# Performance work log

Hardware: AMD Instinct MI355X
Metric: run time of the kernel (lower is better)

## Reference

```python
import jax, jax.numpy as jnp
import numpy as np

B, K, D_MODEL = 64, 256, 512
D_STATE, D_CONV, EXPAND = 16, 4, 1
D_INNER = EXPAND * D_MODEL
DT_RANK = (D_MODEL + 15) // 16  # 32
EPS = 1e-5


def _layer_norm(x, g, b):
    m = jnp.mean(x, axis=-1, keepdims=True)
    v = jnp.mean(jnp.square(x - m), axis=-1, keepdims=True)
    return (x - m) * jax.lax.rsqrt(v + EPS) * g + b


def _silu(x):
    return x * jax.nn.sigmoid(x)


def _mamba_block(x, in_proj_w, conv_w, conv_b, x_proj_w, dt_proj_w, dt_proj_b, A_log, Dp, out_proj_w):
    # x: (B, K, d_model)
    b, k, _ = x.shape
    d_inner = A_log.shape[0]
    d_state = A_log.shape[1]
    dt_rank = dt_proj_w.shape[1]
    xz = x @ in_proj_w.T                      # (B, K, 2*d_inner)
    xi, z = jnp.split(xz, 2, axis=-1)
    # causal depthwise conv1d, width d_conv
    pad = conv_w.shape[1] - 1
    xp = jnp.pad(xi, ((0, 0), (pad, 0), (0, 0)))
    xc = conv_b + sum(xp[:, w:w + k, :] * conv_w[:, w] for w in range(conv_w.shape[1]))
    xc = _silu(xc)
    proj = xc @ x_proj_w.T                    # (B, K, dt_rank + 2*d_state)
    dtr = proj[..., :dt_rank]
    Bc = proj[..., dt_rank:dt_rank + d_state]  # (B, K, d_state)
    Cc = proj[..., dt_rank + d_state:]         # (B, K, d_state)
    dt = jax.nn.softplus(dtr @ dt_proj_w.T + dt_proj_b)  # (B, K, d_inner)
    A = -jnp.exp(A_log)                       # (d_inner, d_state)

    def step(h, inp):
        dt_t, x_t, B_t, C_t = inp             # (B,d_inner),(B,d_inner),(B,d_state),(B,d_state)
        dA = jnp.exp(dt_t[:, :, None] * A)    # (B, d_inner, d_state)
        h = dA * h + (dt_t * x_t)[:, :, None] * B_t[:, None, :]
        y = jnp.einsum('bds,bs->bd', h, C_t)
        return h, y

    h0 = jnp.zeros((b, d_inner, d_state), x.dtype)
    xs = (dt.transpose(1, 0, 2), xc.transpose(1, 0, 2),
          Bc.transpose(1, 0, 2), Cc.transpose(1, 0, 2))
    _, ys = jax.lax.scan(step, h0, xs)        # ys: (K, B, d_inner)
    y = ys.transpose(1, 0, 2) + xc * Dp       # skip term D*x
    y = y * _silu(z)
    return y @ out_proj_w.T


def setup_inputs() -> dict:
    key = jax.random.key(0)
    ks = jax.random.split(key, 8)
    s = 0.02
    slots = jax.random.normal(ks[0], (B, K, D_MODEL), dtype=jnp.float32)
    in_proj_w = jax.random.normal(ks[1], (2 * D_INNER, D_MODEL), jnp.float32) * s
    conv_w = jax.random.normal(ks[2], (D_INNER, D_CONV), jnp.float32) * 0.1
    conv_b = jnp.zeros((D_INNER,), jnp.float32)
    x_proj_w = jax.random.normal(ks[3], (DT_RANK + 2 * D_STATE, D_INNER), jnp.float32) * s
    dt_proj_w = jax.random.normal(ks[4], (D_INNER, DT_RANK), jnp.float32) * s
    dt_proj_b = jax.random.normal(ks[5], (D_INNER,), jnp.float32) * 0.1 - 4.0  # small softplus(dt)
    A_log = jnp.log(jnp.broadcast_to(jnp.arange(1, D_STATE + 1, dtype=jnp.float32), (D_INNER, D_STATE)))
    Dp = jnp.ones((D_INNER,), jnp.float32)
    out_proj_w = jax.random.normal(ks[6], (D_MODEL, D_INNER), jnp.float32) * s
    ln_g = jnp.ones((D_MODEL,), jnp.float32)
    ln_b = jnp.zeros((D_MODEL,), jnp.float32)
    fln_g = jnp.ones((D_MODEL,), jnp.float32)
    fln_b = jnp.zeros((D_MODEL,), jnp.float32)
    return {"slots": slots, "ln_g": ln_g, "ln_b": ln_b,
            "in_proj_w": in_proj_w, "conv_w": conv_w, "conv_b": conv_b,
            "x_proj_w": x_proj_w, "dt_proj_w": dt_proj_w, "dt_proj_b": dt_proj_b,
            "A_log": A_log, "Dp": Dp, "out_proj_w": out_proj_w,
            "fln_g": fln_g, "fln_b": fln_b}


def reference(slots, ln_g, ln_b, in_proj_w, conv_w, conv_b, x_proj_w,
              dt_proj_w, dt_proj_b, A_log, Dp, out_proj_w, fln_g, fln_b):
    x = slots
    # num_layers = 1: pre-norm -> mamba -> residual
    residual = x
    x = _layer_norm(x, ln_g, ln_b)
    x = _mamba_block(x, in_proj_w, conv_w, conv_b, x_proj_w,
                     dt_proj_w, dt_proj_b, A_log, Dp, out_proj_w)
    x = x + residual
    return _layer_norm(x, fln_g, fln_b)
```

## Files before the change

kernel.cpp:

```cpp
#include <hip/hip_runtime.h>
#include <hip/hip_bf16.h>


#define NTOK 16384
#define DM   512

typedef __attribute__((ext_vector_type(8))) short bf16x8;
typedef __attribute__((ext_vector_type(4))) float f32x4;

__device__ __forceinline__ unsigned short f2bf(float f){
  unsigned int u = __float_as_uint(f);
  u = (u + 0x7fffu + ((u >> 16) & 1u)) >> 16;
  return (unsigned short)u;
}
__device__ __forceinline__ float bfu(unsigned short p){ return __uint_as_float(((unsigned int)p) << 16); }
__device__ __forceinline__ unsigned int pk2(float a, float b){
  return (unsigned int)f2bf(a) | ((unsigned int)f2bf(b) << 16);
}
__device__ __forceinline__ float silu(float a){ return a / (1.f + __expf(-a)); }

__device__ __forceinline__ void async_cp16(const unsigned short* g, unsigned short* l){
  __builtin_amdgcn_global_load_lds(
      (const __attribute__((address_space(1))) unsigned int*)g,
      (__attribute__((address_space(3))) unsigned int*)l, 16, 0, 0);
}

__global__ __launch_bounds__(256) void k_cvtw(const float* __restrict__ W,
                                              unsigned short* __restrict__ Wb){
  int i = (blockIdx.x*256 + threadIdx.x)*8;
  float4 a = *(const float4*)(W+i);
  float4 b = *(const float4*)(W+i+4);
  uint4 st = { pk2(a.x,a.y), pk2(a.z,a.w), pk2(b.x,b.y), pk2(b.z,b.w) };
  *(uint4*)(Wb+i) = st;
}

__global__ __launch_bounds__(64) void k_ln(const float* __restrict__ x,
                                           const float* __restrict__ g,
                                           const float* __restrict__ b,
                                           unsigned short* __restrict__ out){
  int tok  = blockIdx.x;
  int lane = threadIdx.x;
  const float* row = x + (size_t)tok*DM + lane*8;
  float4 r0 = *(const float4*)row;
  float4 r1 = *(const float4*)(row + 4);
  float v[8] = {r0.x,r0.y,r0.z,r0.w, r1.x,r1.y,r1.z,r1.w};
  float s = 0.f;
  #pragma unroll
  for (int i=0;i<8;i++) s += v[i];
  #pragma unroll
  for (int o=32;o;o>>=1) s += __shfl_xor(s, o, 64);
  float m = s * (1.0f/512.0f);
  float vs = 0.f;
  #pragma unroll
  for (int i=0;i<8;i++){ float d = v[i]-m; vs += d*d; }
  #pragma unroll
  for (int o=32;o;o>>=1) vs += __shfl_xor(vs, o, 64);
  float rs = rsqrtf(vs*(1.0f/512.0f) + 1e-5f);
  float4 g0 = *(const float4*)(g + lane*8);
  float4 g1 = *(const float4*)(g + lane*8 + 4);
  float4 b0 = *(const float4*)(b + lane*8);
  float4 b1 = *(const float4*)(b + lane*8 + 4);
  float gv[8] = {g0.x,g0.y,g0.z,g0.w, g1.x,g1.y,g1.z,g1.w};
  float bv[8] = {b0.x,b0.y,b0.z,b0.w, b1.x,b1.y,b1.z,b1.w};
  float o8[8];
  #pragma unroll
  for (int i=0;i<8;i++) o8[i] = (v[i]-m)*rs*gv[i] + bv[i];
  uint4 st = { pk2(o8[0],o8[1]), pk2(o8[2],o8[3]), pk2(o8[4],o8[5]), pk2(o8[6],o8[7]) };
  *(uint4*)(out + (size_t)tok*DM + lane*8) = st;
}

__global__ __launch_bounds__(256) void k_gemm(const unsigned short* __restrict__ A,
                                              const unsigned short* __restrict__ Wb,
                                              float* __restrict__ out_f,
                                              unsigned short* __restrict__ out_b,
                                              int mode){
  __shared__ unsigned short As[2][128*32];
  __shared__ unsigned short Bs[2][128*32];
  int t0  = blockIdx.x * 128;
  int n0  = blockIdx.y * 128;
  int tid = threadIdx.x;
  int lane = tid & 63;
  int wv  = tid >> 6;
  int mw  = wv & 1, nw = wv >> 1;
  int m15 = lane & 15, quad = lane >> 4;

  int srow   = wv*32 + (lane >> 2);
  int schunk = ((lane & 3) ^ ((lane >> 3) & 3)) * 8;
  const unsigned short* gA = A  + (size_t)(t0 + srow)*DM + schunk;
  const unsigned short* gB = Wb + (size_t)(n0 + srow)*DM + schunk;
  unsigned short* asb0 = &As[0][(wv*32)*32];
  unsigned short* bsb0 = &Bs[0][(wv*32)*32];
  unsigned short* asb1 = &As[1][(wv*32)*32];
  unsigned short* bsb1 = &Bs[1][(wv*32)*32];

  async_cp16(gA,         asb0);
  async_cp16(gA + 16*DM, asb0 + 16*32);
  async_cp16(gB,         bsb0);
  async_cp16(gB + 16*DM, bsb0 + 16*32);

  f32x4 acc[4][4];
  #pragma unroll
  for (int rb=0;rb<4;rb++)
    #pragma unroll
    for (int cb=0;cb<4;cb++) acc[rb][cb] = (f32x4){0.f,0.f,0.f,0.f};

  int rdsw = (quad ^ ((m15 >> 1) & 3)) * 8;
  int cur = 0;
  for (int ks = 0; ks < 16; ks++){
    __syncthreads();
    if (ks < 15){
      const unsigned short* nA = gA + (ks+1)*32;
      const unsigned short* nB = gB + (ks+1)*32;
      unsigned short* na = cur ? asb0 : asb1;
      unsigned short* nb = cur ? bsb0 : bsb1;
      async_cp16(nA,         na);
      async_cp16(nA + 16*DM, na + 16*32);
      async_cp16(nB,         nb);
      async_cp16(nB + 16*DM, nb + 16*32);
    }
    bf16x8 af[4], bfr[4];
    #pragma unroll
    for (int rb=0;rb<4;rb++)
      af[rb] = *(const bf16x8*)&As[cur][(mw*64 + rb*16 + m15)*32 + rdsw];
    #pragma unroll
    for (int cb=0;cb<4;cb++)
      bfr[cb] = *(const bf16x8*)&Bs[cur][(nw*64 + cb*16 + m15)*32 + rdsw];
    #pragma unroll
    for (int rb=0;rb<4;rb++)
      #pragma unroll
      for (int cb=0;cb<4;cb++)
        acc[rb][cb] = __builtin_amdgcn_mfma_f32_16x16x32_bf16(af[rb], bfr[cb], acc[rb][cb], 0, 0, 0);
    cur ^= 1;
  }

  #pragma unroll
  for (int rb=0;rb<4;rb++){
    int tok0 = t0 + mw*64 + rb*16 + quad*4;
    int b    = tok0 >> 8;
    int tl0  = tok0 & 255;
    #pragma unroll
    for (int cb=0;cb<4;cb++){
      int nn = n0 + nw*64 + cb*16 + m15;
      f32x4 v = acc[rb][cb];
      if (mode == 0){
        if (nn < DM){
          *(f32x4*)(out_f + ((size_t)(b*DM + nn))*256 + tl0) = v;
        } else {
          uint2 z2 = { pk2(silu(v[0]), silu(v[1])), pk2(silu(v[2]), silu(v[3])) };
          *(uint2*)(out_b + ((size_t)(b*DM + (nn - DM)))*256 + tl0) = z2;
        }
      } else {
        #pragma unroll
        for (int r=0;r<4;r++) out_f[(size_t)(tok0+r)*DM + nn] = v[r];
      }
    }
  }
}

__global__ __launch_bounds__(256) void k_xproj(const float* __restrict__ xiT,
                                               const float* __restrict__ cw,
                                               const float* __restrict__ cb,
                                               const unsigned short* __restrict__ xpwb,
                                               const unsigned short* __restrict__ dtwb,
                                               const float* __restrict__ dtb,
                                               float* __restrict__ dtT,
                                               float* __restrict__ Bc,
                                               float* __restrict__ Cc){
  __shared__ unsigned short xcb[32*520];
  __shared__ unsigned short Bst[2][64*32];
  __shared__ unsigned short pjA[32*40];
  int t0  = blockIdx.x * 32;
  int b   = t0 >> 8;
  int tl0 = t0 & 255;
  int tid = threadIdx.x;
  int lane = tid & 63;
  int wv  = tid >> 6;
  int m15 = lane & 15, quad = lane >> 4;

  #pragma unroll
  for (int j=0;j<2;j++){
    int d = tid + 256*j;
    float4 cr = *(const float4*)(cw + d*4);
    float a0 = cb[d];
    const float* row = xiT + ((size_t)(b*DM + d))*256;
    float w[36];
    if (tl0 == 0){
      w[0]=w[1]=w[2]=w[3]=0.f;
      #pragma unroll
      for (int q2=0;q2<8;q2++){
        float4 v4 = *(const float4*)(row + q2*4);
        w[4+q2*4]=v4.x; w[5+q2*4]=v4.y; w[6+q2*4]=v4.z; w[7+q2*4]=v4.w;
      }
    } else {
      const float* p4 = row + tl0 - 4;
      #pragma unroll
      for (int q2=0;q2<9;q2++){
        float4 v4 = *(const float4*)(p4 + q2*4);
        w[q2*4]=v4.x; w[1+q2*4]=v4.y; w[2+q2*4]=v4.z; w[3+q2*4]=v4.w;
      }
    }
    #pragma unroll
    for (int t=0;t<32;t++){
      float a = a0 + w[t+1]*cr.x + w[t+2]*cr.y + w[t+3]*cr.z + w[t+4]*cr.w;
      xcb[t*520 + d] = f2bf(silu(a));
    }
  }

  int srow = wv*16 + (lane >> 2);
  int sch  = ((lane & 3) ^ ((lane >> 3) & 3)) * 8;
  async_cp16(xpwb + srow*DM + sch, &Bst[0][(wv*16)*32]);
  __syncthreads();

  int mt = wv & 1, ntp = wv >> 1;
  f32x4 pacc[2];
  pacc[0] = (f32x4){0.f,0.f,0.f,0.f};
  pacc[1] = (f32x4){0.f,0.f,0.f,0.f};
  int rdsw = (quad ^ ((m15 >> 1) & 3)) * 8;
  int cur = 0;
  for (int ks=0; ks<16; ks++){
    if (ks < 15)
      async_cp16(xpwb + srow*DM + (ks+1)*32 + sch, &Bst[cur^1][(wv*16)*32]);
    bf16x8 af = *(const bf16x8*)&xcb[(mt*16 + m15)*520 + ks*32 + quad*8];
    #pragma unroll
    for (int j2=0;j2<2;j2++){
      int nt = ntp*2 + j2;
      bf16x8 bfr = *(const bf16x8*)&Bst[cur][(nt*16 + m15)*32 + rdsw];
      pacc[j2] = __builtin_amdgcn_mfma_f32_16x16x32_bf16(af, bfr, pacc[j2], 0, 0, 0);
    }
    cur ^= 1;
    __syncthreads();
  }

  if (ntp == 0){
    #pragma unroll
    for (int j2=0;j2<2;j2++){
      int col = j2*16 + m15;
      #pragma unroll
      for (int r=0;r<4;r++)
        pjA[(mt*16 + quad*4 + r)*40 + col] = f2bf(pacc[j2][r]);
    }
  } else {
    #pragma unroll
    for (int j2=0;j2<2;j2++){
      int c = j2*16 + m15;
      #pragma unroll
      for (int r=0;r<4;r++){
        int tt = t0 + mt*16 + quad*4 + r;
        float v = pacc[j2][r];
        if (c < 16) Bc[(size_t)tt*16 + c] = v;
        else        Cc[(size_t)tt*16 + (c-16)] = v;
      }
    }
  }
  __syncthreads();

  bf16x8 adt = *(const bf16x8*)&pjA[(mt*16 + m15)*40 + quad*8];
  int nh = wv >> 1;
  #pragma unroll
  for (int j2=0;j2<16;j2++){
    int nn = (nh*16 + j2)*16 + m15;
    bf16x8 bfr = *(const bf16x8*)(dtwb + nn*32 + quad*8);
    f32x4 dacc = (f32x4){0.f,0.f,0.f,0.f};
    dacc = __builtin_amdgcn_mfma_f32_16x16x32_bf16(adt, bfr, dacc, 0, 0, 0);
    float bb = dtb[nn];
    f32x4 o;
    #pragma unroll
    for (int r=0;r<4;r++){
      float s = dacc[r] + bb;
      o[r] = (s > 20.f) ? s : log1pf(__expf(s));
    }
    *(f32x4*)(dtT + ((size_t)(b*DM + nn))*256 + tl0 + mt*16 + quad*4) = o;
  }
}

__global__ __launch_bounds__(256) void k_scan(const float* __restrict__ dtT,
                                              const float* __restrict__ xiT,
                                              const unsigned short* __restrict__ zsT,
                                              const float* __restrict__ Bc,
                                              const float* __restrict__ Cc,
                                              const float* __restrict__ cw,
                                              const float* __restrict__ cb,
                                              const float* __restrict__ Alog,
                                              const float* __restrict__ Dpw,
                                              unsigned short* __restrict__ ya){
  int tid = threadIdx.x;
  int sl  = tid & 3;
  int q   = blockIdx.x*64 + (tid >> 2);
  int d   = q & 511;
  int b   = q >> 9;
  float4 Alr = *(const float4*)(Alog + d*16 + sl*4);
  float A0 = -__expf(Alr.x), A1 = -__expf(Alr.y);
  float A2 = -__expf(Alr.z), A3 = -__expf(Alr.w);
  float Dv = Dpw[d];
  float4 cr = *(const float4*)(cw + d*4);
  float cbv = cb[d];
  float h0=0.f, h1=0.f, h2=0.f, h3=0.f;
  float xm1=0.f, xm2=0.f, xm3=0.f;
  const float* dtp = dtT + (size_t)q*256;
  const float* xip = xiT + (size_t)q*256;
  const unsigned short* zsp = zsT + (size_t)q*256;
  unsigned short* yap = ya + (size_t)b*256*DM + d;
  const float* Bp = Bc + (size_t)b*4096 + sl*4;
  const float* Cp = Cc + (size_t)b*4096 + sl*4;
  #pragma unroll 2
  for (int t0=0; t0<256; t0+=4){
    float4 dt4 = *(const float4*)(dtp + t0);
    float4 xi4 = *(const float4*)(xip + t0);
    uint2  zz  = *(const uint2*)(zsp + t0);
    float xts[4] = {xi4.x, xi4.y, xi4.z, xi4.w};
    float dvs[4] = {dt4.x, dt4.y, dt4.z, dt4.w};
    float zsf[4] = { bfu((unsigned short)zz.x), bfu((unsigned short)(zz.x>>16)),
                     bfu((unsigned short)zz.y), bfu((unsigned short)(zz.y>>16)) };
    #pragma unroll
    for (int r=0;r<4;r++){
      float4 Bv = *(const float4*)(Bp + (t0+r)*16);
      float4 Cv = *(const float4*)(Cp + (t0+r)*16);
      float a  = cbv + xm3*cr.x + xm2*cr.y + xm1*cr.z + xts[r]*cr.w;
      float u  = silu(a);
      float dv = dvs[r];
      float du = dv*u;
      h0 = __expf(dv*A0)*h0 + du*Bv.x;
      h1 = __expf(dv*A1)*h1 + du*Bv.y;
      h2 = __expf(dv*A2)*h2 + du*Bv.z;
      h3 = __expf(dv*A3)*h3 + du*Bv.w;
      float yy = h0*Cv.x + h1*Cv.y + h2*Cv.z + h3*Cv.w;
      yy += __shfl_xor(yy, 1);
      yy += __shfl_xor(yy, 2);
      if (sl == 0) yap[(size_t)(t0+r)*DM] = f2bf((yy + u*Dv) * zsf[r]);
      xm3 = xm2; xm2 = xm1; xm1 = xts[r];
    }
  }
}

__global__ __launch_bounds__(64) void k_fln(const float* __restrict__ o,
                                            const float* __restrict__ resid,
                                            const float* __restrict__ g,
                                            const float* __restrict__ b,
                                            float* __restrict__ out){
  int tok  = blockIdx.x;
  int lane = threadIdx.x;
  const float* row = o     + (size_t)tok*DM + lane*8;
  const float* rr  = resid + (size_t)tok*DM + lane*8;
  float4 r0 = *(const float4*)row;
  float4 r1 = *(const float4*)(row + 4);
  float4 s0 = *(const float4*)rr;
  float4 s1 = *(const float4*)(rr + 4);
  float v[8] = {r0.x+s0.x, r0.y+s0.y, r0.z+s0.z, r0.w+s0.w,
                r1.x+s1.x, r1.y+s1.y, r1.z+s1.z, r1.w+s1.w};
  float s = 0.f;
  #pragma unroll
  for (int i=0;i<8;i++) s += v[i];
  #pragma unroll
  for (int o2=32;o2;o2>>=1) s += __shfl_xor(s, o2, 64);
  float m = s * (1.0f/512.0f);
  float vs = 0.f;
  #pragma unroll
  for (int i=0;i<8;i++){ float d = v[i]-m; vs += d*d; }
  #pragma unroll
  for (int o2=32;o2;o2>>=1) vs += __shfl_xor(vs, o2, 64);
  float rs = rsqrtf(vs*(1.0f/512.0f) + 1e-5f);
  float4 g0 = *(const float4*)(g + lane*8);
  float4 g1 = *(const float4*)(g + lane*8 + 4);
  float4 b0 = *(const float4*)(b + lane*8);
  float4 b1 = *(const float4*)(b + lane*8 + 4);
  float gv[8] = {g0.x,g0.y,g0.z,g0.w, g1.x,g1.y,g1.z,g1.w};
  float bv[8] = {b0.x,b0.y,b0.z,b0.w, b1.x,b1.y,b1.z,b1.w};
  float o8[8];
  #pragma unroll
  for (int i=0;i<8;i++) o8[i] = (v[i]-m)*rs*gv[i] + bv[i];
  float4* op = (float4*)(out + (size_t)tok*DM + lane*8);
  op[0] = make_float4(o8[0],o8[1],o8[2],o8[3]);
  op[1] = make_float4(o8[4],o8[5],o8[6],o8[7]);
}

extern "C" void kernel_launch(void* const* d_in, const int* in_sizes, int n_in,
                              void* d_out, int out_size, void* d_ws, size_t ws_size,
                              hipStream_t stream) {
  const float* slots     = (const float*)d_in[0];
  const float* ln_g      = (const float*)d_in[1];
  const float* ln_b      = (const float*)d_in[2];
  const float* in_proj_w = (const float*)d_in[3];
  const float* conv_w    = (const float*)d_in[4];
  const float* conv_b    = (const float*)d_in[5];
  const float* x_proj_w  = (const float*)d_in[6];
  const float* dt_proj_w = (const float*)d_in[7];
  const float* dt_proj_b = (const float*)d_in[8];
  const float* A_log     = (const float*)d_in[9];
  const float* Dp        = (const float*)d_in[10];
  const float* out_projw = (const float*)d_in[11];
  const float* fln_g     = (const float*)d_in[12];
  const float* fln_b     = (const float*)d_in[13];
  float* out = (float*)d_out;

  const size_t MB = 1024*1024;
  char* base = (char*)d_ws;
  float*          xiT  = (float*)(base);
  unsigned short* xlnb = (unsigned short*)(base + 32*MB);
  unsigned short* yab  = xlnb;
  unsigned short* xpwb = xlnb;
  unsigned short* dtwb = xlnb + 32768;
  unsigned short* zsT  = (unsigned short*)(base + 48*MB);
  unsigned short* WbO  = zsT;
  float*          dto  = (float*)(base + 64*MB);
  unsigned short* WbI  = (unsigned short*)dto;
  float*          Bc   = (float*)(base + 96*MB);
  float*          Cc   = (float*)(base + 97*MB);

  k_ln   <<<NTOK,           64, 0, stream>>>(slots, ln_g, ln_b, xlnb);
  k_cvtw <<<256,           256, 0, stream>>>(in_proj_w, WbI);
  k_gemm <<<dim3(128, 8),  256, 0, stream>>>(xlnb, WbI, xiT, zsT, 0);
  k_cvtw <<<16,            256, 0, stream>>>(x_proj_w, xpwb);
  k_cvtw <<<8,             256, 0, stream>>>(dt_proj_w, dtwb);
  k_xproj<<<NTOK/32,       256, 0, stream>>>(xiT, conv_w, conv_b, xpwb, dtwb, dt_proj_b,
                                             dto, Bc, Cc);
  k_scan <<<512,           256, 0, stream>>>(dto, xiT, zsT, Bc, Cc, conv_w, conv_b, A_log, Dp, yab);
  k_cvtw <<<128,           256, 0, stream>>>(out_projw, WbO);
  k_gemm <<<dim3(128, 4),  256, 0, stream>>>(yab, WbO, dto, (unsigned short*)0, 1);
  k_fln  <<<NTOK,           64, 0, stream>>>(dto, slots, fln_g, fln_b, out);
}
```

Baseline: 319.6 us.

## Split selective scan into chunked three-pass parallel scan over time

```diff
diff --git a/kernel.cpp b/kernel.cpp
--- a/kernel.cpp
+++ b/kernel.cpp
@@ -18,6 +18,9 @@
   return (unsigned int)f2bf(a) | ((unsigned int)f2bf(b) << 16);
 }
 __device__ __forceinline__ float silu(float a){ return a / (1.f + __expf(-a)); }
+__device__ __forceinline__ float silu_f(float a){
+  return a * __builtin_amdgcn_rcpf(1.f + __expf(-a));
+}
 
 __device__ __forceinline__ void async_cp16(const unsigned short* g, unsigned short* l){
   __builtin_amdgcn_global_load_lds(
@@ -202,7 +205,7 @@
     #pragma unroll
     for (int t=0;t<32;t++){
       float a = a0 + w[t+1]*cr.x + w[t+2]*cr.y + w[t+3]*cr.z + w[t+4]*cr.w;
-      xcb[t*520 + d] = f2bf(silu(a));
+      xcb[t*520 + d] = f2bf(silu_f(a));
     }
   }
 
@@ -273,37 +276,114 @@
   }
 }
 
-__global__ __launch_bounds__(256) void k_scan(const float* __restrict__ dtT,
-                                              const float* __restrict__ xiT,
-                                              const unsigned short* __restrict__ zsT,
-                                              const float* __restrict__ Bc,
-                                              const float* __restrict__ Cc,
-                                              const float* __restrict__ cw,
-                                              const float* __restrict__ cb,
-                                              const float* __restrict__ Alog,
-                                              const float* __restrict__ Dpw,
-                                              unsigned short* __restrict__ ya){
+__global__ __launch_bounds__(256) void k_scan1(const float* __restrict__ dtT,
+                                               const float* __restrict__ xiT,
+                                               const float* __restrict__ Bc,
+                                               const float* __restrict__ cw,
+                                               const float* __restrict__ cb,
+                                               const float* __restrict__ Alog,
+                                               float* __restrict__ PL){
   int tid = threadIdx.x;
   int sl  = tid & 3;
-  int q   = blockIdx.x*64 + (tid >> 2);
+  int blk = blockIdx.x;
+  int c   = blk & 3;
+  int q   = (blk >> 2)*64 + (tid >> 2);
   int d   = q & 511;
   int b   = q >> 9;
+  int tl0 = c*64;
+  float4 Alr = *(const float4*)(Alog + d*16 + sl*4);
+  float A0 = -__expf(Alr.x), A1 = -__expf(Alr.y);
+  float A2 = -__expf(Alr.z), A3 = -__expf(Alr.w);
+  float4 cr = *(const float4*)(cw + d*4);
+  float cbv = cb[d];
+  const float* dtp = dtT + (size_t)q*256;
+  const float* xip = xiT + (size_t)q*256;
+  const float* Bp  = Bc + (size_t)b*4096 + sl*4;
+  float xm1, xm2, xm3;
+  if (c == 0){ xm1 = xm2 = xm3 = 0.f; }
+  else { float4 xw = *(const float4*)(xip + tl0 - 4); xm3 = xw.y; xm2 = xw.z; xm1 = xw.w; }
+  float h0=0.f,h1=0.f,h2=0.f,h3=0.f;
+  float p0=1.f,p1=1.f,p2=1.f,p3=1.f;
+  #pragma unroll 2
+  for (int t0=tl0; t0<tl0+64; t0+=4){
+    float4 dt4 = *(const float4*)(dtp + t0);
+    float4 xi4 = *(const float4*)(xip + t0);
+    float xts[4] = {xi4.x, xi4.y, xi4.z, xi4.w};
+    float dvs[4] = {dt4.x, dt4.y, dt4.z, dt4.w};
+    #pragma unroll
+    for (int r=0;r<4;r++){
+      float4 Bv = *(const float4*)(Bp + (t0+r)*16);
+      float a  = cbv + xm3*cr.x + xm2*cr.y + xm1*cr.z + xts[r]*cr.w;
+      float u  = silu_f(a);
+      float dv = dvs[r];
+      float du = dv*u;
+      float e0 = __expf(dv*A0), e1 = __expf(dv*A1);
+      float e2 = __expf(dv*A2), e3 = __expf(dv*A3);
+      h0 = e0*h0 + du*Bv.x;  p0 *= e0;
+      h1 = e1*h1 + du*Bv.y;  p1 *= e1;
+      h2 = e2*h2 + du*Bv.z;  p2 *= e2;
+      h3 = e3*h3 + du*Bv.w;  p3 *= e3;
+      xm3 = xm2; xm2 = xm1; xm1 = xts[r];
+    }
+  }
+  float* p = PL + (((size_t)q*4 + c)*32 + sl*8);
+  *(f32x4*)p       = (f32x4){p0,p1,p2,p3};
+  *(f32x4*)(p + 4) = (f32x4){h0,h1,h2,h3};
+}
+
+__global__ __launch_bounds__(256) void k_scan2(const float* __restrict__ PL,
+                                               float* __restrict__ h0buf){
+  int i = blockIdx.x*256 + threadIdx.x;
+  int q = i >> 2, sl = i & 3;
+  const float* p = PL + ((size_t)q*4)*32 + sl*8;
+  f32x4 h = (f32x4){0.f,0.f,0.f,0.f};
+  #pragma unroll
+  for (int c=0;c<4;c++){
+    *(f32x4*)(h0buf + (((size_t)q*4 + c)*16 + sl*4)) = h;
+    f32x4 P = *(const f32x4*)(p + c*32);
+    f32x4 L = *(const f32x4*)(p + c*32 + 4);
+    h = L + P*h;
+  }
+}
+
+__global__ __launch_bounds__(256) void k_scan3(const float* __restrict__ dtT,
+                                               const float* __restrict__ xiT,
+                                               const unsigned short* __restrict__ zsT,
+                                               const float* __restrict__ Bc,
+                                               const float* __restrict__ Cc,
+                                               const float* __restrict__ cw,
+                                               const float* __restrict__ cb,
+                                               const float* __restrict__ Alog,
+                                               const float* __restrict__ Dpw,
+                                               const float* __restrict__ h0buf,
+                                               unsigned short* __restrict__ ya){
+  int tid = threadIdx.x;
+  int sl  = tid & 3;
+  int blk = blockIdx.x;
+  int c   = blk & 3;
+  int q   = (blk >> 2)*64 + (tid >> 2);
+  int d   = q & 511;
+  int b   = q >> 9;
+  int tl0 = c*64;
   float4 Alr = *(const float4*)(Alog + d*16 + sl*4);
   float A0 = -__expf(Alr.x), A1 = -__expf(Alr.y);
   float A2 = -__expf(Alr.z), A3 = -__expf(Alr.w);
   float Dv = Dpw[d];
   float4 cr = *(const float4*)(cw + d*4);
   float cbv = cb[d];
-  float h0=0.f, h1=0.f, h2=0.f, h3=0.f;
-  float xm1=0.f, xm2=0.f, xm3=0.f;
   const float* dtp = dtT + (size_t)q*256;
   const float* xip = xiT + (size_t)q*256;
   const unsigned short* zsp = zsT + (size_t)q*256;
   unsigned short* yap = ya + (size_t)b*256*DM + d;
   const float* Bp = Bc + (size_t)b*4096 + sl*4;
   const float* Cp = Cc + (size_t)b*4096 + sl*4;
+  float xm1, xm2, xm3;
+  if (c == 0){ xm1 = xm2 = xm3 = 0.f; }
+  else { float4 xw = *(const float4*)(xip + tl0 - 4); xm3 = xw.y; xm2 = xw.z; xm1 = xw.w; }
+  f32x4 hi = *(const f32x4*)(h0buf + (((size_t)q*4 + c)*16 + sl*4));
+  float h0 = hi[0], h1 = hi[1], h2 = hi[2], h3 = hi[3];
   #pragma unroll 2
-  for (int t0=0; t0<256; t0+=4){
+  for (int t0=tl0; t0<tl0+64; t0+=4){
     float4 dt4 = *(const float4*)(dtp + t0);
     float4 xi4 = *(const float4*)(xip + t0);
     uint2  zz  = *(const uint2*)(zsp + t0);
@@ -316,7 +396,7 @@
       float4 Bv = *(const float4*)(Bp + (t0+r)*16);
       float4 Cv = *(const float4*)(Cp + (t0+r)*16);
       float a  = cbv + xm3*cr.x + xm2*cr.y + xm1*cr.z + xts[r]*cr.w;
-      float u  = silu(a);
+      float u  = silu_f(a);
       float dv = dvs[r];
       float du = dv*u;
       h0 = __expf(dv*A0)*h0 + du*Bv.x;
@@ -406,6 +486,9 @@
   float*          Bc   = (float*)(base + 96*MB);
   float*          Cc   = (float*)(base + 97*MB);
 
+  float* PL    = out;
+  float* h0buf = out + (size_t)4*1024*1024;
+
   k_ln   <<<NTOK,           64, 0, stream>>>(slots, ln_g, ln_b, xlnb);
   k_cvtw <<<256,           256, 0, stream>>>(in_proj_w, WbI);
   k_gemm <<<dim3(128, 8),  256, 0, stream>>>(xlnb, WbI, xiT, zsT, 0);
@@ -413,7 +496,10 @@
   k_cvtw <<<8,             256, 0, stream>>>(dt_proj_w, dtwb);
   k_xproj<<<NTOK/32,       256, 0, stream>>>(xiT, conv_w, conv_b, xpwb, dtwb, dt_proj_b,
                                              dto, Bc, Cc);
-  k_scan <<<512,           256, 0, stream>>>(dto, xiT, zsT, Bc, Cc, conv_w, conv_b, A_log, Dp, yab);
+  k_scan1<<<2048,          256, 0, stream>>>(dto, xiT, Bc, conv_w, conv_b, A_log, PL);
+  k_scan2<<<512,           256, 0, stream>>>(PL, h0buf);
+  k_scan3<<<2048,          256, 0, stream>>>(dto, xiT, zsT, Bc, Cc, conv_w, conv_b, A_log, Dp,
+                                             h0buf, yab);
   k_cvtw <<<128,           256, 0, stream>>>(out_projw, WbO);
   k_gemm <<<dim3(128, 4),  256, 0, stream>>>(yab, WbO, dto, (unsigned short*)0, 1);
   k_fln  <<<NTOK,           64, 0, stream>>>(dto, slots, fln_g, fln_b, out);
```

Measured after the change: 466.8 us. +46.0%, slower.
